# Kernel tuning notes

Hardware: AMD Instinct MI355X
Metric: run time of the kernel (lower is better)

Reference implementation:

```python
import jax, jax.numpy as jnp
import numpy as np

BATCH, SEQ, D_MODEL = 4, 8192, 2048
NUM_HEADS, NUM_RATES = 32, 6
HEAD_DIM = D_MODEL // NUM_HEADS


def setup_inputs() -> dict:
    key = jax.random.key(0)
    x = jax.random.normal(key, (BATCH, SEQ, D_MODEL), dtype=jnp.float32)
    return {"x": x}


def reference(x) -> jnp.ndarray:
    B, L, D = x.shape
    H, hd = NUM_HEADS, HEAD_DIM
    scale = 1.0 / jnp.sqrt(jnp.asarray(hd, x.dtype))
    outputs = jnp.zeros((B, L, D), dtype=x.dtype)
    denoms = jnp.zeros((B, L, H), dtype=x.dtype)
    for i in range(NUM_RATES):
        dil = 2 ** i          # dilation rate
        seg = 2 ** i          # segment size
        n = L // dil // seg   # segments per dilation offset
        # gather all dilation offsets at once: (B, dil, L//dil, D)
        xo = x.reshape(B, L // dil, dil, D).transpose(0, 2, 1, 3)
        # split into segments and heads: (B, dil, n, seg, H, hd)
        xs = xo.reshape(B, dil, n, seg, H, hd)
        scores = jnp.einsum('bonqhd,bonkhd->bonhqk', xs * scale, xs)
        probs = jax.nn.softmax(scores, axis=-1)
        out = jnp.einsum('bonhqk,bonkhd->bonqhd', probs, xs)
        # per-query softmax denominator (stable): (B, dil, n, seg, H)
        den = jnp.swapaxes(jnp.exp(jax.nn.logsumexp(scores, axis=-1)), -1, -2)
        # scatter-add back onto the full sequence (inverse of the strided gather)
        out_full = out.reshape(B, dil, L // dil, D).transpose(0, 2, 1, 3).reshape(B, L, D)
        den_full = den.reshape(B, dil, L // dil, H).transpose(0, 2, 1, 3).reshape(B, L, H)
        outputs = outputs + out_full
        denoms = denoms + den_full
    # softmax-weighted combine over heads (per token), broadcast over head_dim
    w = jax.nn.softmax(denoms, axis=-1)  # (B, L, H)
    return (outputs.reshape(B, L, H, hd) * w[..., None]).reshape(B, L, D)
```

## Files before the change

kernel.cpp:

```cpp
#include <hip/hip_runtime.h>

#define B_   4
#define L_   8192
#define D_   2048
#define H_   32
#define WIN_ 1024
#define U_   512
#define PAD_ 68
#define QSC  0.125f

template <int CTRL>
__device__ __forceinline__ float dpp_add(float v) {
    int s = __builtin_amdgcn_update_dpp(0, __builtin_bit_cast(int, v), CTRL, 0xf, 0xf, true);
    return v + __builtin_bit_cast(float, s);
}
__device__ __forceinline__ float red8(float v) {
    v = dpp_add<0xB1>(v);
    v = dpp_add<0x4E>(v);
    v = dpp_add<0x141>(v);
    return v;
}

__device__ __forceinline__ float dot8(const float4& a0, const float4& a1,
                                      const float4& b0, const float4& b1) {
    float s = a0.x * b0.x, t = a0.y * b0.y;
    s = fmaf(a0.z, b0.z, s); t = fmaf(a0.w, b0.w, t);
    s = fmaf(a1.x, b1.x, s); t = fmaf(a1.y, b1.y, t);
    s = fmaf(a1.z, b1.z, s); t = fmaf(a1.w, b1.w, t);
    return s + t;
}

__device__ __forceinline__ void fma4(float4& a, float s, const float4& b) {
    a.x = fmaf(s, b.x, a.x); a.y = fmaf(s, b.y, a.y);
    a.z = fmaf(s, b.z, a.z); a.w = fmaf(s, b.w, a.w);
}

__device__ __forceinline__ float4 mul4(const float4& a, float s) {
    return make_float4(a.x * s, a.y * s, a.z * s, a.w * s);
}

__global__ __launch_bounds__(1024)
void ddattn_k1(const float* __restrict__ x, float* __restrict__ out,
               float* __restrict__ den) {
    const int bid = blockIdx.x;
    const int h   = bid & 31;
    const int p   = (bid >> 5) & 1;
    const int win = (bid >> 6) & 7;
    const int b   = bid >> 9;

    __shared__ float Xs[U_ * PAD_];
    const int t0 = win * WIN_;
    const float* xb = x + ((size_t)b * L_ + (size_t)(t0 + p)) * D_ + h * 64;

    for (int idx = threadIdx.x; idx < U_ * 16; idx += 1024) {
        const int row = idx >> 4, c = idx & 15;
        *(float4*)(&Xs[row * PAD_ + c * 4]) =
            *(const float4*)(xb + (size_t)row * (2 * D_) + c * 4);
    }
    __syncthreads();

    const int lane8 = threadIdx.x & 7;
    const int slot  = threadIdx.x >> 3;
    const int off   = lane8 * 8;

#pragma unroll 1
    for (int qq = 0; qq < 4; qq++) {
        const int u = qq * 128 + slot;

        float4 acc0 = *(const float4*)(&Xs[u * PAD_ + off]);
        float4 acc1 = *(const float4*)(&Xs[u * PAD_ + off + 4]);
        const float4 Qs0 = mul4(acc0, QSC), Qs1 = mul4(acc1, QSC);
        float dn = __expf(red8(dot8(Qs0, Qs1, acc0, acc1)));

#pragma unroll
        for (int i = 1; i <= 5; i++) {
            const int step = 1 << (i - 1), cnt = 1 << i;
            const int ub = ((u >> (2 * i - 1)) << (2 * i - 1)) | (u & (step - 1));
            const float* ptr = &Xs[ub * PAD_ + off];
            float4 E0 = make_float4(0, 0, 0, 0), E1 = E0;
            float D = 0.f;
#pragma unroll 4
            for (int k = 0; k < cnt; k++) {
                const float4 R0 = *(const float4*)(ptr);
                const float4 R1 = *(const float4*)(ptr + 4);
                ptr += step * PAD_;
                const float e = __expf(red8(dot8(Qs0, Qs1, R0, R1)));
                D += e;
                fma4(E0, e, R0); fma4(E1, e, R1);
            }
            dn += D;
            const float inv = 1.0f / D;
            fma4(acc0, inv, E0); fma4(acc1, inv, E1);
        }

        const int t = t0 + 2 * u + p;
        float* op = out + ((size_t)b * L_ + t) * D_ + h * 64 + off;
        *(float4*)op = acc0; *(float4*)(op + 4) = acc1;
        if (lane8 == 0) den[((size_t)b * L_ + t) * H_ + h] = dn;
    }
}

__global__ __launch_bounds__(256)
void ddattn_k2(float* __restrict__ out, const float* __restrict__ den) {
    const int tok0 = blockIdx.x * 2;
    __shared__ float sden[2][H_];
    __shared__ float w2[2][H_];
    if (threadIdx.x < 64)
        sden[threadIdx.x >> 5][threadIdx.x & 31] = den[(size_t)tok0 * H_ + threadIdx.x];
    __syncthreads();
    if (threadIdx.x < 64) {
        const int tt = threadIdx.x >> 5, hh = threadIdx.x & 31;
        float mx = -3.4e38f;
#pragma unroll
        for (int k = 0; k < H_; k++) mx = fmaxf(mx, sden[tt][k]);
        float s = 0.f;
#pragma unroll
        for (int k = 0; k < H_; k++) s += __expf(sden[tt][k] - mx);
        w2[tt][hh] = __expf(sden[tt][hh] - mx) / s;
    }
    __syncthreads();

    float4* o4 = (float4*)(out + (size_t)tok0 * D_);
#pragma unroll
    for (int c = 0; c < 4; c++) {
        const int idx = threadIdx.x + 256 * c;
        const float w = w2[idx >> 9][(idx >> 4) & 31];
        float4 vv = o4[idx];
        vv.x *= w; vv.y *= w; vv.z *= w; vv.w *= w;
        o4[idx] = vv;
    }
}

extern "C" void kernel_launch(void* const* d_in, const int* in_sizes, int n_in,
                              void* d_out, int out_size, void* d_ws, size_t ws_size,
                              hipStream_t stream) {
    const float* x = (const float*)d_in[0];
    float* out = (float*)d_out;
    float* den = (float*)d_ws;

    ddattn_k1<<<dim3(B_ * (L_ / WIN_) * 2 * H_), dim3(1024), 0, stream>>>(x, out, den);
    ddattn_k2<<<dim3(B_ * L_ / 2), dim3(256), 0, stream>>>(out, den);
}
```

Baseline: 784.6 us.

## Remap query-to-wave assignment and split head-softmax combine into two kernels

Changes the query index mapping in the attention kernel so each wavefront covers strided queries, altering the LDS bank and work-distribution pattern. Replaces the combine kernel with a per-token softmax kernel that writes normalized weights in place, plus a bulk scaling kernel with larger per-block work. This drops the shared-memory and syncthreads overhead of the old combine, at the cost of an extra launch and an extra pass over the denominator buffer.

```diff
diff --git a/kernel.cpp b/kernel.cpp
--- a/kernel.cpp
+++ b/kernel.cpp
@@ -62,10 +62,12 @@
     const int lane8 = threadIdx.x & 7;
     const int slot  = threadIdx.x >> 3;
     const int off   = lane8 * 8;
+    const int wv    = slot >> 3;
+    const int j8    = slot & 7;
 
 #pragma unroll 1
     for (int qq = 0; qq < 4; qq++) {
-        const int u = qq * 128 + slot;
+        const int u = wv + 16 * j8 + 128 * qq;
 
         float4 acc0 = *(const float4*)(&Xs[u * PAD_ + off]);
         float4 acc1 = *(const float4*)(&Xs[u * PAD_ + off + 4]);
@@ -101,32 +103,41 @@
 }
 
 __global__ __launch_bounds__(256)
-void ddattn_k2(float* __restrict__ out, const float* __restrict__ den) {
-    const int tok0 = blockIdx.x * 2;
-    __shared__ float sden[2][H_];
-    __shared__ float w2[2][H_];
-    if (threadIdx.x < 64)
-        sden[threadIdx.x >> 5][threadIdx.x & 31] = den[(size_t)tok0 * H_ + threadIdx.x];
-    __syncthreads();
-    if (threadIdx.x < 64) {
-        const int tt = threadIdx.x >> 5, hh = threadIdx.x & 31;
-        float mx = -3.4e38f;
+void ddattn_k2a(float* __restrict__ den) {
+    const int t = blockIdx.x * 256 + threadIdx.x;
+    float* dp = den + (size_t)t * H_;
+    float4 v[8];
+    float mx = -3.4e38f;
 #pragma unroll
-        for (int k = 0; k < H_; k++) mx = fmaxf(mx, sden[tt][k]);
-        float s = 0.f;
+    for (int i = 0; i < 8; i++) {
+        v[i] = *(float4*)(dp + i * 4);
+        mx = fmaxf(mx, fmaxf(fmaxf(v[i].x, v[i].y), fmaxf(v[i].z, v[i].w)));
+    }
+    float s = 0.f;
 #pragma unroll
-        for (int k = 0; k < H_; k++) s += __expf(sden[tt][k] - mx);
-        w2[tt][hh] = __expf(sden[tt][hh] - mx) / s;
+    for (int i = 0; i < 8; i++) {
+        v[i].x = __expf(v[i].x - mx); v[i].y = __expf(v[i].y - mx);
+        v[i].z = __expf(v[i].z - mx); v[i].w = __expf(v[i].w - mx);
+        s += v[i].x + v[i].y + v[i].z + v[i].w;
     }
-    __syncthreads();
+    const float inv = 1.f / s;
+#pragma unroll
+    for (int i = 0; i < 8; i++) {
+        v[i].x *= inv; v[i].y *= inv; v[i].z *= inv; v[i].w *= inv;
+        *(float4*)(dp + i * 4) = v[i];
+    }
+}
 
-    float4* o4 = (float4*)(out + (size_t)tok0 * D_);
-#pragma unroll
-    for (int c = 0; c < 4; c++) {
-        const int idx = threadIdx.x + 256 * c;
-        const float w = w2[idx >> 9][(idx >> 4) & 31];
+__global__ __launch_bounds__(256)
+void ddattn_k2b(float* __restrict__ out, const float* __restrict__ w) {
+    const size_t base = (size_t)blockIdx.x * 8192 + threadIdx.x;
+    float4* o4 = (float4*)out;
+#pragma unroll 4
+    for (int c = 0; c < 32; c++) {
+        const size_t idx = base + (size_t)c * 256;
+        const float ww = w[idx >> 4];
         float4 vv = o4[idx];
-        vv.x *= w; vv.y *= w; vv.z *= w; vv.w *= w;
+        vv.x *= ww; vv.y *= ww; vv.z *= ww; vv.w *= ww;
         o4[idx] = vv;
     }
 }
@@ -139,5 +150,6 @@
     float* den = (float*)d_ws;
 
     ddattn_k1<<<dim3(B_ * (L_ / WIN_) * 2 * H_), dim3(1024), 0, stream>>>(x, out, den);
-    ddattn_k2<<<dim3(B_ * L_ / 2), dim3(256), 0, stream>>>(out, den);
+    ddattn_k2a<<<dim3(B_ * L_ / 256), dim3(256), 0, stream>>>(den);
+    ddattn_k2b<<<dim3(2048), dim3(256), 0, stream>>>(out, den);
 }
```

Result: no change. 794.4 us (+1.2%).
